# Kernel tuning notes

Hardware: AMD Instinct MI355X
Metric: run time of the kernel (lower is better)

Reference implementation:

```python
import jax, jax.numpy as jnp
import numpy as np

B, T, D = 4, 1024, 1024   # batch, block_size, d_model
H, HS = 16, 64            # n_head, head_size


def setup_inputs() -> dict:
    key = jax.random.key(0)
    ks = jax.random.split(key, 6)
    s = 0.02  # small init like nn.Linear default scale
    return {
        "x": jax.random.normal(ks[0], (B, T, D), jnp.float32),
        "Wq": jax.random.normal(ks[1], (H, D, HS), jnp.float32) * s,
        "Wk": jax.random.normal(ks[2], (H, D, HS), jnp.float32) * s,
        "Wv": jax.random.normal(ks[3], (H, D, HS), jnp.float32) * s,
        "Wo": jax.random.normal(ks[4], (H * HS, D), jnp.float32) * s,
        "bo": jnp.zeros((D,), jnp.float32),
    }


def reference(x, Wq, Wk, Wv, Wo, bo):
    # Batched equivalent of the per-head loop: all heads in one einsum.
    q = jnp.einsum('btd,hde->bhte', x, Wq)   # [B,H,T,HS]
    k = jnp.einsum('btd,hde->bhte', x, Wk)
    v = jnp.einsum('btd,hde->bhte', x, Wv)
    scores = jnp.einsum('bhte,bhse->bhts', q, k) * (HS ** -0.5)  # [B,H,T,T]
    causal = jnp.tril(jnp.ones((T, T), dtype=bool))
    scores = jnp.where(causal, scores, -jnp.inf)
    att = jax.nn.softmax(scores, axis=-1)
    out = jnp.einsum('bhts,bhse->bhte', att, v)                  # [B,H,T,HS]
    out = out.transpose(0, 2, 1, 3).reshape(B, T, H * HS)        # concat heads
    return out @ Wo + bo                                         # proj to d_model
```

## Files before the change

### kernel.cpp

```cpp
#include <hip/hip_runtime.h>
#include <math.h>

#define NB 4
#define SEQ 1024
#define DM 1024
#define NH 16
#define HS 64

typedef __attribute__((ext_vector_type(8))) short short8;
typedef __attribute__((ext_vector_type(4))) short short4v;
typedef __attribute__((ext_vector_type(4))) float floatx4;

#define MFMA(a, b, c) __builtin_amdgcn_mfma_f32_16x16x32_bf16((a), (b), (c), 0, 0, 0)

static __device__ __forceinline__ unsigned short f2bf(float f) {
  unsigned int u = __float_as_uint(f);
  u += 0x7FFFu + ((u >> 16) & 1u);
  return (unsigned short)(u >> 16);
}

static __device__ __forceinline__ void g2l(const unsigned short* g, short* l) {
  __builtin_amdgcn_global_load_lds(
      (const __attribute__((address_space(1))) void*)g,
      (__attribute__((address_space(3))) void*)l, 16, 0, 0);
}

#define SWZ_SRC(tid) ((((tid) & 7) ^ (((tid) >> 3) & 7)) << 3)
#define SWZ_RD(B, r) ((((B) ^ ((r) & 7)) << 3))

__global__ __launch_bounds__(256) void prep_all(
    const float* __restrict__ x,
    const float* __restrict__ Wq, const float* __restrict__ Wk,
    const float* __restrict__ Wv, const float* __restrict__ Wo,
    unsigned short* __restrict__ xb,
    unsigned short* __restrict__ Wtq, unsigned short* __restrict__ Wtk,
    unsigned short* __restrict__ Wtv, unsigned short* __restrict__ Wot) {
  __shared__ __align__(16) short Ts[64 * 72];
  const int tid = threadIdx.x;
  const int mat = blockIdx.y;
  if (mat == 4) {
    int base = blockIdx.x * 4096;
#pragma unroll
    for (int i = 0; i < 16; i++) {
      int idx4 = base + tid + i * 256;
      float4 v = *(const float4*)(x + (size_t)idx4 * 4);
      short4v o;
      o[0] = (short)f2bf(v.x); o[1] = (short)f2bf(v.y);
      o[2] = (short)f2bf(v.z); o[3] = (short)f2bf(v.w);
      *(short4v*)(xb + (size_t)idx4 * 4) = o;
    }
    return;
  }
  const float* src;
  unsigned short* dst;
  int r0, c0;
  if (mat < 3) {
    src = (mat == 0) ? Wq : (mat == 1) ? Wk : Wv;
    dst = (mat == 0) ? Wtq : (mat == 1) ? Wtk : Wtv;
    int h = blockIdx.x >> 4;
    int d0 = (blockIdx.x & 15) * 64;
    src += (size_t)(h * DM + d0) * HS;
    dst += (size_t)(h * HS) * DM + d0;
    r0 = HS;  c0 = DM;
  } else {
    src = Wo; dst = Wot;
    int k0 = (blockIdx.x >> 4) * 64;
    int n0 = (blockIdx.x & 15) * 64;
    src += (size_t)k0 * DM + n0;
    dst += (size_t)n0 * DM + k0;
    r0 = DM;  c0 = DM;
  }
#pragma unroll
  for (int i = 0; i < 4; i++) {
    int p = tid + i * 256;
    int row = p >> 4, c4 = (p & 15) << 2;
    float4 v = *(const float4*)(src + (size_t)row * r0 + c4);
    Ts[(c4 + 0) * 72 + row] = (short)f2bf(v.x);
    Ts[(c4 + 1) * 72 + row] = (short)f2bf(v.y);
    Ts[(c4 + 2) * 72 + row] = (short)f2bf(v.z);
    Ts[(c4 + 3) * 72 + row] = (short)f2bf(v.w);
  }
  __syncthreads();
#pragma unroll
  for (int i = 0; i < 2; i++) {
    int p = tid + i * 256;
    int row = p >> 3, c8 = (p & 7) << 3;
    *(short8*)(dst + (size_t)row * c0 + c8) = *(const short8*)&Ts[row * 72 + c8];
  }
}

__global__ __launch_bounds__(256, 3) void qkv_gemm128(
    const unsigned short* __restrict__ xb,
    const unsigned short* __restrict__ Wcat,
    unsigned short* __restrict__ qo,
    unsigned short* __restrict__ ko,
    unsigned short* __restrict__ vo) {
  __shared__ __align__(16) short As[128 * 64];
  __shared__ __align__(16) short Bs[128 * 64];
  const int tid = threadIdx.x;
  const int bm = blockIdx.x, bn = blockIdx.y;
  const int lane = tid & 63, wave = tid >> 6;
  const int quad = lane >> 4, l16 = lane & 15;
  const int wr = wave >> 1, wc = wave & 1;
  const int l7 = l16 & 7;
  const floatx4 fzero = {0.f, 0.f, 0.f, 0.f};

  floatx4 acc[4][4];
#pragma unroll
  for (int i = 0; i < 4; i++)
#pragma unroll
    for (int j = 0; j < 4; j++) acc[i][j] = fzero;

  const int srow = tid >> 3;
  const int scolw = SWZ_SRC(tid);
  const unsigned short* Ag = xb + (size_t)(bm * 128 + srow) * DM + scolw;
  const unsigned short* Bg = Wcat + (size_t)(bn * 128 + srow) * DM + scolw;
  short* Ad = As + tid * 8;
  short* Bd = Bs + tid * 8;

  for (int k0 = 0; k0 < DM; k0 += 64) {
    __syncthreads();
#pragma unroll
    for (int i = 0; i < 4; i++) g2l(Ag + (size_t)i * 32 * DM + k0, Ad + i * 2048);
#pragma unroll
    for (int i = 0; i < 4; i++) g2l(Bg + (size_t)i * 32 * DM + k0, Bd + i * 2048);
    __syncthreads();

    short8 af[4][2], bf[4][2];
#pragma unroll
    for (int ti = 0; ti < 4; ti++)
#pragma unroll
      for (int kh = 0; kh < 2; kh++)
        af[ti][kh] = *(const short8*)&As[(wr * 64 + ti * 16 + l16) * 64 +
                                          SWZ_RD(kh * 4 + quad, l7)];
#pragma unroll
    for (int tj = 0; tj < 4; tj++)
#pragma unroll
      for (int kh = 0; kh < 2; kh++)
        bf[tj][kh] = *(const short8*)&Bs[(wc * 64 + tj * 16 + l16) * 64 +
                                          SWZ_RD(kh * 4 + quad, l7)];
#pragma unroll
    for (int ti = 0; ti < 4; ti++)
#pragma unroll
      for (int tj = 0; tj < 4; tj++) {
        acc[ti][tj] = MFMA(af[ti][0], bf[tj][0], acc[ti][tj]);
        acc[ti][tj] = MFMA(af[ti][1], bf[tj][1], acc[ti][tj]);
      }
  }

  const int mat = bn >> 3;
  const int mbase = bm * 128 + wr * 64 + quad * 4;
  const int nn0 = (bn & 7) * 128 + wc * 64;
  if (mat < 2) {
    unsigned short* dst = (mat == 0) ? qo : ko;
#pragma unroll
    for (int ti = 0; ti < 4; ti++)
#pragma unroll
      for (int tj = 0; tj < 4; tj++) {
        int ecol = nn0 + tj * 16 + l16;
        int h = ecol >> 6, e = ecol & 63;
#pragma unroll
        for (int r = 0; r < 4; r++) {
          int m = mbase + ti * 16 + r;
          int b = m >> 10, t = m & (SEQ - 1);
          dst[((size_t)(b * NH + h) * SEQ + t) * HS + e] = f2bf(acc[ti][tj][r]);
        }
      }
  } else {
#pragma unroll
    for (int ti = 0; ti < 4; ti++)
#pragma unroll
      for (int tj = 0; tj < 4; tj++) {
        int ecol = nn0 + tj * 16 + l16;
        int h = ecol >> 6, e = ecol & 63;
        int m0 = mbase + ti * 16;
        int b = m0 >> 10, t0 = m0 & (SEQ - 1);
        short4v pv;
#pragma unroll
        for (int r = 0; r < 4; r++) pv[r] = (short)f2bf(acc[ti][tj][r]);
        *(short4v*)&vo[((size_t)(b * NH + h) * HS + e) * SEQ + t0] = pv;
      }
  }
}

__global__ __launch_bounds__(256) void attn_kernel(
    const unsigned short* __restrict__ q,
    const unsigned short* __restrict__ k,
    const unsigned short* __restrict__ v,
    unsigned short* __restrict__ o)
{
  __shared__ __align__(16) short Qs[128 * 64];
  __shared__ __align__(16) short Ks[2][64 * 64];
  __shared__ __align__(16) short Vt[2][64 * 64];
  __shared__ __align__(16) short Ps[128 * 76];
  const int tid = threadIdx.x;
  const int lid = (int)blockIdx.x;
  const int jj = lid & 3, half = lid >> 8, pp = (lid >> 2) & 63;
  const int qt = half ? jj : 7 - jj;
  const int h = pp & 15, b = pp >> 4;
  const int lane = tid & 63, wave = tid >> 6;
  const int quad = lane >> 4, l16 = lane & 15;
  const int l7 = l16 & 7;
  const size_t bh = (size_t)(b * NH + h) * SEQ * HS;
  const unsigned short* qp = q + bh + (size_t)qt * 128 * HS;
  const unsigned short* kbase = k + bh;
  const unsigned short* vbase = v + (size_t)(b * NH + h) * HS * SEQ;
  const floatx4 fzero = {0.f, 0.f, 0.f, 0.f};
  const float c2 = 0.125f * 1.44269504089f;
  const float C0 = 16.0f * 1.44269504089f;
  const int srow = tid >> 3;
  const int scolw = SWZ_SRC(tid);

#pragma unroll
  for (int i = 0; i < 4; i++)
    g2l(qp + (size_t)(srow + i * 32) * HS + scolw, Qs + tid * 8 + i * 2048);
  {
    const unsigned short* kp = kbase;
#pragma unroll
    for (int i = 0; i < 2; i++)
      g2l(kp + (size_t)(srow + i * 32) * HS + scolw, &Ks[0][tid * 8 + i * 2048]);
#pragma unroll
    for (int i = 0; i < 2; i++)
      g2l(vbase + (size_t)(srow + i * 32) * SEQ + scolw, &Vt[0][tid * 8 + i * 2048]);
  }
  __syncthreads();
  short8 qa[2][2];
#pragma unroll
  for (int ih = 0; ih < 2; ih++)
#pragma unroll
    for (int kh = 0; kh < 2; kh++)
      qa[ih][kh] = *(const short8*)&Qs[(wave * 32 + ih * 16 + l16) * 64 +
                                        SWZ_RD(kh * 4 + quad, l7)];

  const int rowbase = qt * 128 + wave * 32;
  float l_[2][4];
  floatx4 O[2][4];
#pragma unroll
  for (int ih = 0; ih < 2; ih++)
#pragma unroll
    for (int r = 0; r < 4; r++) l_[ih][r] = 0.f;
#pragma unroll
  for (int ih = 0; ih < 2; ih++)
#pragma unroll
    for (int tj = 0; tj < 4; tj++) O[ih][tj] = fzero;

  const int ktmax = 2 * qt + 1;
  for (int kt = 0; kt <= ktmax; kt++) {
    const int cur = kt & 1;
    if (kt < ktmax) {
      const unsigned short* kp = kbase + (size_t)(kt + 1) * 64 * HS;
#pragma unroll
      for (int i = 0; i < 2; i++)
        g2l(kp + (size_t)(srow + i * 32) * HS + scolw,
            &Ks[1 - cur][tid * 8 + i * 2048]);
#pragma unroll
      for (int i = 0; i < 2; i++)
        g2l(vbase + (size_t)(srow + i * 32) * SEQ + (kt + 1) * 64 + scolw,
            &Vt[1 - cur][tid * 8 + i * 2048]);
    }

    if (kt * 64 <= rowbase + 31) {
      floatx4 S[2][4];
#pragma unroll
      for (int tj = 0; tj < 4; tj++) {
        short8 b0 = *(const short8*)&Ks[cur][(tj * 16 + l16) * 64 + SWZ_RD(quad, l7)];
        short8 b1 = *(const short8*)&Ks[cur][(tj * 16 + l16) * 64 + SWZ_RD(4 + quad, l7)];
#pragma unroll
        for (int ih = 0; ih < 2; ih++) {
          floatx4 s = fzero;
          s = MFMA(qa[ih][0], b0, s);
          s = MFMA(qa[ih][1], b1, s);
          S[ih][tj] = s;
        }
      }
      if (kt * 64 + 63 > rowbase) {
#pragma unroll
        for (int ih = 0; ih < 2; ih++)
#pragma unroll
          for (int tj = 0; tj < 4; tj++) {
            int col = kt * 64 + tj * 16 + l16;
#pragma unroll
            for (int r = 0; r < 4; r++) {
              int row = rowbase + ih * 16 + quad * 4 + r;
              if (col > row) S[ih][tj][r] = -INFINITY;
            }
          }
      }
#pragma unroll
      for (int ih = 0; ih < 2; ih++)
#pragma unroll
        for (int tj = 0; tj < 4; tj++)
#pragma unroll
          for (int r = 0; r < 4; r++) {
            float pv = __builtin_amdgcn_exp2f(S[ih][tj][r] * c2 - C0);
            S[ih][tj][r] = pv;
            l_[ih][r] += pv;
          }
#pragma unroll
      for (int ih = 0; ih < 2; ih++)
#pragma unroll
        for (int tj = 0; tj < 4; tj++)
#pragma unroll
          for (int r = 0; r < 4; r++)
            Ps[(wave * 32 + ih * 16 + quad * 4 + r) * 76 + tj * 16 + l16] =
                (short)f2bf(S[ih][tj][r]);

      short8 pa[2][2];
#pragma unroll
      for (int ih = 0; ih < 2; ih++)
#pragma unroll
        for (int kh = 0; kh < 2; kh++)
          pa[ih][kh] = *(const short8*)&Ps[(wave * 32 + ih * 16 + l16) * 76 +
                                            kh * 32 + quad * 8];
#pragma unroll
      for (int tj = 0; tj < 4; tj++) {
        short8 b0 = *(const short8*)&Vt[cur][(tj * 16 + l16) * 64 + SWZ_RD(quad, l7)];
        short8 b1 = *(const short8*)&Vt[cur][(tj * 16 + l16) * 64 + SWZ_RD(4 + quad, l7)];
#pragma unroll
        for (int ih = 0; ih < 2; ih++) {
          O[ih][tj] = MFMA(pa[ih][0], b0, O[ih][tj]);
          O[ih][tj] = MFMA(pa[ih][1], b1, O[ih][tj]);
        }
      }
    }
    __syncthreads();
  }

#pragma unroll
  for (int ih = 0; ih < 2; ih++)
#pragma unroll
    for (int r = 0; r < 4; r++) {
      float lsum = l_[ih][r];
#pragma unroll
      for (int off = 1; off < 16; off <<= 1)
        lsum += __shfl_xor(lsum, off, 16);
      float inv = 1.0f / lsum;
      int t = qt * 128 + wave * 32 + ih * 16 + quad * 4 + r;
#pragma unroll
      for (int tj = 0; tj < 4; tj++) {
        int e = tj * 16 + l16;
        o[((size_t)(b * SEQ + t)) * DM + h * HS + e] = f2bf(O[ih][tj][r] * inv);
      }
    }
}

__global__ __launch_bounds__(256, 3) void out_gemm64(
    const unsigned short* __restrict__ A,
    const unsigned short* __restrict__ Bt,
    const float* __restrict__ bo,
    float* __restrict__ out) {
  __shared__ __align__(16) short As[128 * 64];
  __shared__ __align__(16) short Bs[64 * 64];
  const int tid = threadIdx.x;
  const int bm = blockIdx.x, bn = blockIdx.y;
  const int lane = tid & 63, wave = tid >> 6;
  const int quad = lane >> 4, l16 = lane & 15;
  const int wr = wave >> 1, wc = wave & 1;
  const int l7 = l16 & 7;
  const floatx4 fzero = {0.f, 0.f, 0.f, 0.f};

  floatx4 acc[4][2];
#pragma unroll
  for (int i = 0; i < 4; i++)
#pragma unroll
    for (int j = 0; j < 2; j++) acc[i][j] = fzero;

  const int srow = tid >> 3;
  const int scolw = SWZ_SRC(tid);
  const unsigned short* Ag = A + (size_t)(bm * 128 + srow) * DM + scolw;
  const unsigned short* Bg = Bt + (size_t)(bn * 64 + srow) * DM + scolw;
  short* Ad = As + tid * 8;
  short* Bd = Bs + tid * 8;

  for (int k0 = 0; k0 < DM; k0 += 64) {
    __syncthreads();
#pragma unroll
    for (int i = 0; i < 4; i++) g2l(Ag + (size_t)i * 32 * DM + k0, Ad + i * 2048);
#pragma unroll
    for (int i = 0; i < 2; i++) g2l(Bg + (size_t)i * 32 * DM + k0, Bd + i * 2048);
    __syncthreads();

    short8 af[4][2], bf[2][2];
#pragma unroll
    for (int ti = 0; ti < 4; ti++)
#pragma unroll
      for (int kh = 0; kh < 2; kh++)
        af[ti][kh] = *(const short8*)&As[(wr * 64 + ti * 16 + l16) * 64 +
                                          SWZ_RD(kh * 4 + quad, l7)];
#pragma unroll
    for (int tj = 0; tj < 2; tj++)
#pragma unroll
      for (int kh = 0; kh < 2; kh++)
        bf[tj][kh] = *(const short8*)&Bs[(wc * 32 + tj * 16 + l16) * 64 +
                                          SWZ_RD(kh * 4 + quad, l7)];
#pragma unroll
    for (int ti = 0; ti < 4; ti++)
#pragma unroll
      for (int tj = 0; tj < 2; tj++) {
        acc[ti][tj] = MFMA(af[ti][0], bf[tj][0], acc[ti][tj]);
        acc[ti][tj] = MFMA(af[ti][1], bf[tj][1], acc[ti][tj]);
      }
  }

#pragma unroll
  for (int ti = 0; ti < 4; ti++)
#pragma unroll
    for (int tj = 0; tj < 2; tj++) {
      int n = bn * 64 + wc * 32 + tj * 16 + l16;
      float bias = bo[n];
#pragma unroll
      for (int r = 0; r < 4; r++) {
        int m = bm * 128 + wr * 64 + ti * 16 + quad * 4 + r;
        out[(size_t)m * DM + n] = acc[ti][tj][r] + bias;
      }
    }
}

extern "C" void kernel_launch(void* const* d_in, const int* in_sizes, int n_in,
                              void* d_out, int out_size, void* d_ws, size_t ws_size,
                              hipStream_t stream) {
  const float* x  = (const float*)d_in[0];
  const float* Wq = (const float*)d_in[1];
  const float* Wk = (const float*)d_in[2];
  const float* Wv = (const float*)d_in[3];
  const float* Wo = (const float*)d_in[4];
  const float* bo = (const float*)d_in[5];
  float* out = (float*)d_out;

  const size_t nx = (size_t)NB * SEQ * DM;
  const size_t nw = (size_t)DM * DM;
  unsigned short* xb  = (unsigned short*)d_ws;
  unsigned short* wtq = xb + nx;
  unsigned short* wtk = wtq + nw;
  unsigned short* wtv = wtk + nw;
  unsigned short* wot = wtv + nw;
  unsigned short* qws = wot + nw;
  unsigned short* kws = qws + nx;
  unsigned short* vws = kws + nx;
  unsigned short* aws = vws + nx;

  dim3 blk(256);
  prep_all<<<dim3(256, 5), blk, 0, stream>>>(x, Wq, Wk, Wv, Wo,
                                             xb, wtq, wtk, wtv, wot);
  qkv_gemm128<<<dim3(32, 24), blk, 0, stream>>>(xb, wtq, qws, kws, vws);
  attn_kernel<<<dim3(512), blk, 0, stream>>>(qws, kws, vws, aws);
  out_gemm64<<<dim3(32, 16), blk, 0, stream>>>(aws, wot, bo, out);
}
```

Measured before the change: 157.5 us.

## Replace direct global-to-LDS loads with register-staged prefetch pipelining

All three kernels stop using global_load_lds and instead load the next K/V or GEMM tile into registers before computing on the current one. The registers are written to LDS after the MFMA work. This overlaps global memory latency with compute in the single-buffered GEMMs, which before had to wait on each synchronous load. The launch_bounds occupancy hint of 3 is also dropped, which adds register pressure from the staging registers and may reduce occupancy.

```diff
diff --git a/kernel.cpp b/kernel.cpp
--- a/kernel.cpp
+++ b/kernel.cpp
@@ -89,7 +89,7 @@
   }
 }
 
-__global__ __launch_bounds__(256, 3) void qkv_gemm128(
+__global__ __launch_bounds__(256) void qkv_gemm128(
     const unsigned short* __restrict__ xb,
     const unsigned short* __restrict__ Wcat,
     unsigned short* __restrict__ qo,
@@ -118,13 +118,28 @@
   short* Ad = As + tid * 8;
   short* Bd = Bs + tid * 8;
 
+  int4 ra[4], rb[4];
+#pragma unroll
+  for (int i = 0; i < 4; i++) {
+    ra[i] = *(const int4*)(Ag + (size_t)i * 32 * DM);
+    rb[i] = *(const int4*)(Bg + (size_t)i * 32 * DM);
+  }
+#pragma unroll
+  for (int i = 0; i < 4; i++) {
+    *(int4*)(Ad + i * 2048) = ra[i];
+    *(int4*)(Bd + i * 2048) = rb[i];
+  }
+  __syncthreads();
+
   for (int k0 = 0; k0 < DM; k0 += 64) {
-    __syncthreads();
-#pragma unroll
-    for (int i = 0; i < 4; i++) g2l(Ag + (size_t)i * 32 * DM + k0, Ad + i * 2048);
-#pragma unroll
-    for (int i = 0; i < 4; i++) g2l(Bg + (size_t)i * 32 * DM + k0, Bd + i * 2048);
-    __syncthreads();
+    const bool more = (k0 + 64) < DM;
+    if (more) {
+#pragma unroll
+      for (int i = 0; i < 4; i++) {
+        ra[i] = *(const int4*)(Ag + (size_t)i * 32 * DM + k0 + 64);
+        rb[i] = *(const int4*)(Bg + (size_t)i * 32 * DM + k0 + 64);
+      }
+    }
 
     short8 af[4][2], bf[4][2];
 #pragma unroll
@@ -146,6 +161,16 @@
         acc[ti][tj] = MFMA(af[ti][0], bf[tj][0], acc[ti][tj]);
         acc[ti][tj] = MFMA(af[ti][1], bf[tj][1], acc[ti][tj]);
       }
+
+    if (more) {
+      __syncthreads();
+#pragma unroll
+      for (int i = 0; i < 4; i++) {
+        *(int4*)(Ad + i * 2048) = ra[i];
+        *(int4*)(Bd + i * 2048) = rb[i];
+      }
+      __syncthreads();
+    }
   }
 
   const int mat = bn >> 3;
@@ -215,13 +240,17 @@
   for (int i = 0; i < 4; i++)
     g2l(qp + (size_t)(srow + i * 32) * HS + scolw, Qs + tid * 8 + i * 2048);
   {
-    const unsigned short* kp = kbase;
-#pragma unroll
-    for (int i = 0; i < 2; i++)
-      g2l(kp + (size_t)(srow + i * 32) * HS + scolw, &Ks[0][tid * 8 + i * 2048]);
-#pragma unroll
-    for (int i = 0; i < 2; i++)
-      g2l(vbase + (size_t)(srow + i * 32) * SEQ + scolw, &Vt[0][tid * 8 + i * 2048]);
+    int4 rk0[2], rv0[2];
+#pragma unroll
+    for (int i = 0; i < 2; i++) {
+      rk0[i] = *(const int4*)(kbase + (size_t)(srow + i * 32) * HS + scolw);
+      rv0[i] = *(const int4*)(vbase + (size_t)(srow + i * 32) * SEQ + scolw);
+    }
+#pragma unroll
+    for (int i = 0; i < 2; i++) {
+      *(int4*)&Ks[0][tid * 8 + i * 2048] = rk0[i];
+      *(int4*)&Vt[0][tid * 8 + i * 2048] = rv0[i];
+    }
   }
   __syncthreads();
   short8 qa[2][2];
@@ -247,16 +276,16 @@
   const int ktmax = 2 * qt + 1;
   for (int kt = 0; kt <= ktmax; kt++) {
     const int cur = kt & 1;
-    if (kt < ktmax) {
+    int4 rk[2], rv[2];
+    const bool more = kt < ktmax;
+    if (more) {
       const unsigned short* kp = kbase + (size_t)(kt + 1) * 64 * HS;
 #pragma unroll
-      for (int i = 0; i < 2; i++)
-        g2l(kp + (size_t)(srow + i * 32) * HS + scolw,
-            &Ks[1 - cur][tid * 8 + i * 2048]);
-#pragma unroll
-      for (int i = 0; i < 2; i++)
-        g2l(vbase + (size_t)(srow + i * 32) * SEQ + (kt + 1) * 64 + scolw,
-            &Vt[1 - cur][tid * 8 + i * 2048]);
+      for (int i = 0; i < 2; i++) {
+        rk[i] = *(const int4*)(kp + (size_t)(srow + i * 32) * HS + scolw);
+        rv[i] = *(const int4*)(vbase + (size_t)(srow + i * 32) * SEQ +
+                               (kt + 1) * 64 + scolw);
+      }
     }
 
     if (kt * 64 <= rowbase + 31) {
@@ -323,6 +352,14 @@
         }
       }
     }
+
+    if (more) {
+#pragma unroll
+      for (int i = 0; i < 2; i++) {
+        *(int4*)&Ks[1 - cur][tid * 8 + i * 2048] = rk[i];
+        *(int4*)&Vt[1 - cur][tid * 8 + i * 2048] = rv[i];
+      }
+    }
     __syncthreads();
   }
 
@@ -344,7 +381,7 @@
     }
 }
 
-__global__ __launch_bounds__(256, 3) void out_gemm64(
+__global__ __launch_bounds__(256) void out_gemm64(
     const unsigned short* __restrict__ A,
     const unsigned short* __restrict__ Bt,
     const float* __restrict__ bo,
@@ -372,13 +409,27 @@
   short* Ad = As + tid * 8;
   short* Bd = Bs + tid * 8;
 
+  int4 ra[4], rb[2];
+#pragma unroll
+  for (int i = 0; i < 4; i++) ra[i] = *(const int4*)(Ag + (size_t)i * 32 * DM);
+#pragma unroll
+  for (int i = 0; i < 2; i++) rb[i] = *(const int4*)(Bg + (size_t)i * 32 * DM);
+#pragma unroll
+  for (int i = 0; i < 4; i++) *(int4*)(Ad + i * 2048) = ra[i];
+#pragma unroll
+  for (int i = 0; i < 2; i++) *(int4*)(Bd + i * 2048) = rb[i];
+  __syncthreads();
+
   for (int k0 = 0; k0 < DM; k0 += 64) {
-    __syncthreads();
-#pragma unroll
-    for (int i = 0; i < 4; i++) g2l(Ag + (size_t)i * 32 * DM + k0, Ad + i * 2048);
-#pragma unroll
-    for (int i = 0; i < 2; i++) g2l(Bg + (size_t)i * 32 * DM + k0, Bd + i * 2048);
-    __syncthreads();
+    const bool more = (k0 + 64) < DM;
+    if (more) {
+#pragma unroll
+      for (int i = 0; i < 4; i++)
+        ra[i] = *(const int4*)(Ag + (size_t)i * 32 * DM + k0 + 64);
+#pragma unroll
+      for (int i = 0; i < 2; i++)
+        rb[i] = *(const int4*)(Bg + (size_t)i * 32 * DM + k0 + 64);
+    }
 
     short8 af[4][2], bf[2][2];
 #pragma unroll
@@ -400,6 +451,15 @@
         acc[ti][tj] = MFMA(af[ti][0], bf[tj][0], acc[ti][tj]);
         acc[ti][tj] = MFMA(af[ti][1], bf[tj][1], acc[ti][tj]);
       }
+
+    if (more) {
+      __syncthreads();
+#pragma unroll
+      for (int i = 0; i < 4; i++) *(int4*)(Ad + i * 2048) = ra[i];
+#pragma unroll
+      for (int i = 0; i < 2; i++) *(int4*)(Bd + i * 2048) = rb[i];
+      __syncthreads();
+    }
   }
 
 #pragma unroll
```

Measured after the change: 285.9 us. 1.82x slower.

## Split attention block across 8 waves with 16 query rows each

Applied to the files above, without the earlier changes.

The attention kernel now runs 512 threads (8 waves) per block instead of 256, and each wave handles 16 query rows instead of 32. Loads of Q/K/V tiles are spread over twice as many threads, and per-wave register state (S, O, P fragments) is halved. This aims to raise latency hiding and shorten per-wave work, including better causal skipping at 16-row granularity. The cost is that K/V LDS reads are duplicated across more waves and more threads share each barrier.

```diff
diff --git a/kernel.cpp b/kernel.cpp
--- a/kernel.cpp
+++ b/kernel.cpp
@@ -183,7 +183,7 @@
   }
 }
 
-__global__ __launch_bounds__(256) void attn_kernel(
+__global__ __launch_bounds__(512) void attn_kernel(
     const unsigned short* __restrict__ q,
     const unsigned short* __restrict__ k,
     const unsigned short* __restrict__ v,
@@ -212,136 +212,102 @@
   const int scolw = SWZ_SRC(tid);
 
 #pragma unroll
-  for (int i = 0; i < 4; i++)
-    g2l(qp + (size_t)(srow + i * 32) * HS + scolw, Qs + tid * 8 + i * 2048);
-  {
-    const unsigned short* kp = kbase;
-#pragma unroll
-    for (int i = 0; i < 2; i++)
-      g2l(kp + (size_t)(srow + i * 32) * HS + scolw, &Ks[0][tid * 8 + i * 2048]);
-#pragma unroll
-    for (int i = 0; i < 2; i++)
-      g2l(vbase + (size_t)(srow + i * 32) * SEQ + scolw, &Vt[0][tid * 8 + i * 2048]);
-  }
+  for (int i = 0; i < 2; i++)
+    g2l(qp + (size_t)(srow + i * 64) * HS + scolw, Qs + tid * 8 + i * 4096);
+  g2l(kbase + (size_t)srow * HS + scolw, &Ks[0][tid * 8]);
+  g2l(vbase + (size_t)srow * SEQ + scolw, &Vt[0][tid * 8]);
   __syncthreads();
-  short8 qa[2][2];
-#pragma unroll
-  for (int ih = 0; ih < 2; ih++)
-#pragma unroll
-    for (int kh = 0; kh < 2; kh++)
-      qa[ih][kh] = *(const short8*)&Qs[(wave * 32 + ih * 16 + l16) * 64 +
-                                        SWZ_RD(kh * 4 + quad, l7)];
-
-  const int rowbase = qt * 128 + wave * 32;
-  float l_[2][4];
-  floatx4 O[2][4];
-#pragma unroll
-  for (int ih = 0; ih < 2; ih++)
-#pragma unroll
-    for (int r = 0; r < 4; r++) l_[ih][r] = 0.f;
-#pragma unroll
-  for (int ih = 0; ih < 2; ih++)
-#pragma unroll
-    for (int tj = 0; tj < 4; tj++) O[ih][tj] = fzero;
+
+  short8 qa[2];
+#pragma unroll
+  for (int kh = 0; kh < 2; kh++)
+    qa[kh] = *(const short8*)&Qs[(wave * 16 + l16) * 64 +
+                                  SWZ_RD(kh * 4 + quad, l7)];
+
+  const int rowbase = qt * 128 + wave * 16;
+  float l_[4];
+  floatx4 O[4];
+#pragma unroll
+  for (int r = 0; r < 4; r++) l_[r] = 0.f;
+#pragma unroll
+  for (int tj = 0; tj < 4; tj++) O[tj] = fzero;
 
   const int ktmax = 2 * qt + 1;
   for (int kt = 0; kt <= ktmax; kt++) {
     const int cur = kt & 1;
     if (kt < ktmax) {
-      const unsigned short* kp = kbase + (size_t)(kt + 1) * 64 * HS;
-#pragma unroll
-      for (int i = 0; i < 2; i++)
-        g2l(kp + (size_t)(srow + i * 32) * HS + scolw,
-            &Ks[1 - cur][tid * 8 + i * 2048]);
-#pragma unroll
-      for (int i = 0; i < 2; i++)
-        g2l(vbase + (size_t)(srow + i * 32) * SEQ + (kt + 1) * 64 + scolw,
-            &Vt[1 - cur][tid * 8 + i * 2048]);
+      g2l(kbase + (size_t)(kt + 1) * 64 * HS + (size_t)srow * HS + scolw,
+          &Ks[1 - cur][tid * 8]);
+      g2l(vbase + (size_t)srow * SEQ + (kt + 1) * 64 + scolw,
+          &Vt[1 - cur][tid * 8]);
     }
 
-    if (kt * 64 <= rowbase + 31) {
-      floatx4 S[2][4];
+    if (kt * 64 <= rowbase + 15) {
+      floatx4 S[4];
 #pragma unroll
       for (int tj = 0; tj < 4; tj++) {
         short8 b0 = *(const short8*)&Ks[cur][(tj * 16 + l16) * 64 + SWZ_RD(quad, l7)];
         short8 b1 = *(const short8*)&Ks[cur][(tj * 16 + l16) * 64 + SWZ_RD(4 + quad, l7)];
-#pragma unroll
-        for (int ih = 0; ih < 2; ih++) {
-          floatx4 s = fzero;
-          s = MFMA(qa[ih][0], b0, s);
-          s = MFMA(qa[ih][1], b1, s);
-          S[ih][tj] = s;
+        floatx4 s = fzero;
+        s = MFMA(qa[0], b0, s);
+        s = MFMA(qa[1], b1, s);
+        S[tj] = s;
+      }
+      if (kt * 64 + 63 > rowbase) {
+#pragma unroll
+        for (int tj = 0; tj < 4; tj++) {
+          int col = kt * 64 + tj * 16 + l16;
+#pragma unroll
+          for (int r = 0; r < 4; r++) {
+            int row = rowbase + quad * 4 + r;
+            if (col > row) S[tj][r] = -INFINITY;
+          }
         }
       }
-      if (kt * 64 + 63 > rowbase) {
-#pragma unroll
-        for (int ih = 0; ih < 2; ih++)
-#pragma unroll
-          for (int tj = 0; tj < 4; tj++) {
-            int col = kt * 64 + tj * 16 + l16;
-#pragma unroll
-            for (int r = 0; r < 4; r++) {
-              int row = rowbase + ih * 16 + quad * 4 + r;
-              if (col > row) S[ih][tj][r] = -INFINITY;
-            }
-          }
-      }
-#pragma unroll
-      for (int ih = 0; ih < 2; ih++)
-#pragma unroll
-        for (int tj = 0; tj < 4; tj++)
-#pragma unroll
-          for (int r = 0; r < 4; r++) {
-            float pv = __builtin_amdgcn_exp2f(S[ih][tj][r] * c2 - C0);
-            S[ih][tj][r] = pv;
-            l_[ih][r] += pv;
-          }
-#pragma unroll
-      for (int ih = 0; ih < 2; ih++)
-#pragma unroll
-        for (int tj = 0; tj < 4; tj++)
-#pragma unroll
-          for (int r = 0; r < 4; r++)
-            Ps[(wave * 32 + ih * 16 + quad * 4 + r) * 76 + tj * 16 + l16] =
-                (short)f2bf(S[ih][tj][r]);
-
-      short8 pa[2][2];
-#pragma unroll
-      for (int ih = 0; ih < 2; ih++)
-#pragma unroll
-        for (int kh = 0; kh < 2; kh++)
-          pa[ih][kh] = *(const short8*)&Ps[(wave * 32 + ih * 16 + l16) * 76 +
-                                            kh * 32 + quad * 8];
+#pragma unroll
+      for (int tj = 0; tj < 4; tj++)
+#pragma unroll
+        for (int r = 0; r < 4; r++) {
+          float pv = __builtin_amdgcn_exp2f(S[tj][r] * c2 - C0);
+          S[tj][r] = pv;
+          l_[r] += pv;
+        }
+#pragma unroll
+      for (int tj = 0; tj < 4; tj++)
+#pragma unroll
+        for (int r = 0; r < 4; r++)
+          Ps[(wave * 16 + quad * 4 + r) * 76 + tj * 16 + l16] =
+              (short)f2bf(S[tj][r]);
+
+      short8 pa[2];
+#pragma unroll
+      for (int kh = 0; kh < 2; kh++)
+        pa[kh] = *(const short8*)&Ps[(wave * 16 + l16) * 76 + kh * 32 + quad * 8];
 #pragma unroll
       for (int tj = 0; tj < 4; tj++) {
         short8 b0 = *(const short8*)&Vt[cur][(tj * 16 + l16) * 64 + SWZ_RD(quad, l7)];
         short8 b1 = *(const short8*)&Vt[cur][(tj * 16 + l16) * 64 + SWZ_RD(4 + quad, l7)];
-#pragma unroll
-        for (int ih = 0; ih < 2; ih++) {
-          O[ih][tj] = MFMA(pa[ih][0], b0, O[ih][tj]);
-          O[ih][tj] = MFMA(pa[ih][1], b1, O[ih][tj]);
-        }
+        O[tj] = MFMA(pa[0], b0, O[tj]);
+        O[tj] = MFMA(pa[1], b1, O[tj]);
       }
     }
     __syncthreads();
   }
 
 #pragma unroll
-  for (int ih = 0; ih < 2; ih++)
-#pragma unroll
-    for (int r = 0; r < 4; r++) {
-      float lsum = l_[ih][r];
-#pragma unroll
-      for (int off = 1; off < 16; off <<= 1)
-        lsum += __shfl_xor(lsum, off, 16);
-      float inv = 1.0f / lsum;
-      int t = qt * 128 + wave * 32 + ih * 16 + quad * 4 + r;
-#pragma unroll
-      for (int tj = 0; tj < 4; tj++) {
-        int e = tj * 16 + l16;
-        o[((size_t)(b * SEQ + t)) * DM + h * HS + e] = f2bf(O[ih][tj][r] * inv);
-      }
+  for (int r = 0; r < 4; r++) {
+    float lsum = l_[r];
+#pragma unroll
+    for (int off = 1; off < 16; off <<= 1)
+      lsum += __shfl_xor(lsum, off, 16);
+    float inv = 1.0f / lsum;
+    int t = qt * 128 + wave * 16 + quad * 4 + r;
+#pragma unroll
+    for (int tj = 0; tj < 4; tj++) {
+      int e = tj * 16 + l16;
+      o[((size_t)(b * SEQ + t)) * DM + h * HS + e] = f2bf(O[tj][r] * inv);
     }
+  }
 }
 
 __global__ __launch_bounds__(256, 3) void out_gemm64(
@@ -439,10 +405,9 @@
   unsigned short* vws = kws + nx;
   unsigned short* aws = vws + nx;
 
-  dim3 blk(256);
-  prep_all<<<dim3(256, 5), blk, 0, stream>>>(x, Wq, Wk, Wv, Wo,
-                                             xb, wtq, wtk, wtv, wot);
-  qkv_gemm128<<<dim3(32, 24), blk, 0, stream>>>(xb, wtq, qws, kws, vws);
-  attn_kernel<<<dim3(512), blk, 0, stream>>>(qws, kws, vws, aws);
-  out_gemm64<<<dim3(32, 16), blk, 0, stream>>>(aws, wot, bo, out);
-}
+  prep_all<<<dim3(256, 5), dim3(256), 0, stream>>>(x, Wq, Wk, Wv, Wo,
+                                                   xb, wtq, wtk, wtv, wot);
+  qkv_gemm128<<<dim3(32, 24), dim3(256), 0, stream>>>(xb, wtq, qws, kws, vws);
+  attn_kernel<<<dim3(512), dim3(512), 0, stream>>>(qws, kws, vws, aws);
+  out_gemm64<<<dim3(32, 16), dim3(256), 0, stream>>>(aws, wot, bo, out);
+}
```

Result: no change. 155.5 us (-1.3%).
